# Performance work log

Hardware: AMD Instinct MI355X
Metric: run time of the kernel (lower is better)

Reference implementation:

```python
import jax, jax.numpy as jnp
import numpy as np

N, D, K = 32768, 256, 8192
SQRT3 = 3.0 ** 0.5


def setup_inputs() -> dict:
    key = jax.random.key(0)
    k1, k2 = jax.random.split(key)
    x = jax.random.normal(k1, (N, D), dtype=jnp.float32)
    # torch .uniform_(-sqrt(3), sqrt(3)) on an [D, K] table
    embeddings = jax.random.uniform(k2, (D, K), dtype=jnp.float32,
                                    minval=-SQRT3, maxval=SQRT3)
    return {"x": x, "embeddings": embeddings}


def reference(x, embeddings):
    # x: [N, D] (forward flattens from dim 1; 2D input is identity)
    # embeddings: [D, K]
    # squared L2 distances: ||y||^2 - 2 y.E + ||e||^2  -> [N, K]
    dist = (jnp.sum(x * x, axis=1, keepdims=True)
            - 2.0 * (x @ embeddings)
            + jnp.sum(embeddings * embeddings, axis=0, keepdims=True))
    idx = jnp.argmin(dist, axis=1)  # [N]
    # one_hot(idx) @ E^T == gather of columns of E (same math, no dense one-hot)
    quantized = jnp.take(embeddings, idx, axis=1).T  # [N, D]
    return quantized.reshape(x.shape)
```

## Files before the change

### kernel.cpp

```cpp
#include <hip/hip_runtime.h>
#include <math.h>
#include <float.h>

#define N_ROWS 32768
#define D_DIM  256
#define K_DIM  8192

#define EPS1 0.25f
#define EPS2 0.02f
#define T2CAP 4096
#define T3CAP 512
#define NSPLIT3 16

typedef _Float16 f16;
typedef _Float16 f16x8 __attribute__((ext_vector_type(8)));
typedef float f32x4 __attribute__((ext_vector_type(4)));

#define KSPLIT 8
#define COLS_PER_SPLIT (K_DIM / KSPLIT)
#define CHUNK_COLS 32
#define NCHUNK (COLS_PER_SPLIT / CHUNK_COLS)

__global__ void convx_kernel(const float* __restrict__ X, f16* __restrict__ X16) {
    const size_t i = ((size_t)blockIdx.x * 256 + threadIdx.x) * 8;
    float4 a = *reinterpret_cast<const float4*>(X + i);
    float4 b = *reinterpret_cast<const float4*>(X + i + 4);
    f16x8 o;
    o[0]=(f16)a.x; o[1]=(f16)a.y; o[2]=(f16)a.z; o[3]=(f16)a.w;
    o[4]=(f16)b.x; o[5]=(f16)b.y; o[6]=(f16)b.z; o[7]=(f16)b.w;
    *reinterpret_cast<f16x8*>(X16 + i) = o;
}

__global__ void transpose_kernel(const float* __restrict__ E, float* __restrict__ ET) {
    __shared__ float t[64][65];
    const int bk = blockIdx.x & (K_DIM / 64 - 1);
    const int bd = blockIdx.x >> 7;
    const int c  = threadIdx.x & 63;
    const int r0 = (threadIdx.x >> 6) * 16;
    const int d0 = bd * 64, k0 = bk * 64;
#pragma unroll
    for (int i = 0; i < 16; ++i)
        t[r0 + i][c] = E[(size_t)(d0 + r0 + i) * K_DIM + k0 + c];
    __syncthreads();
#pragma unroll
    for (int i = 0; i < 16; ++i)
        ET[(size_t)(k0 + r0 + i) * D_DIM + d0 + c] = t[c][r0 + i];
}

__global__ void packe_et_kernel(const float* __restrict__ ET, f16* __restrict__ Epack) {
    const int gid = blockIdx.x * 256 + threadIdx.x;
    const int l    = gid & 63;
    const int t    = (gid >> 6) & 7;
    const int tile = gid >> 9;
    const int k  = 16 * tile + (l & 15);
    const int d0 = 32 * t + (l >> 4) * 8;
    float4 a = *reinterpret_cast<const float4*>(&ET[(size_t)k * D_DIM + d0]);
    float4 b = *reinterpret_cast<const float4*>(&ET[(size_t)k * D_DIM + d0 + 4]);
    f16x8 o;
    o[0]=(f16)a.x; o[1]=(f16)a.y; o[2]=(f16)a.z; o[3]=(f16)a.w;
    o[4]=(f16)b.x; o[5]=(f16)b.y; o[6]=(f16)b.z; o[7]=(f16)b.w;
    *reinterpret_cast<f16x8*>(Epack + (size_t)gid * 8) = o;
}

__global__ void packe_kernel(const float* __restrict__ E, f16* __restrict__ Epack) {
    const int gid = blockIdx.x * 256 + threadIdx.x;
    const int l    = gid & 63;
    const int t    = (gid >> 6) & 7;
    const int tile = gid >> 9;
    const int k  = 16 * tile + (l & 15);
    const int d0 = 32 * t + (l >> 4) * 8;
    f16x8 o;
#pragma unroll
    for (int j = 0; j < 8; ++j) o[j] = (f16)E[(size_t)(d0 + j) * K_DIM + k];
    *reinterpret_cast<f16x8*>(Epack + (size_t)gid * 8) = o;
}

__global__ void nhen_kernel(const float* __restrict__ E, float* __restrict__ nhen) {
    const int k = blockIdx.x * 256 + threadIdx.x;
    float s = 0.0f;
#pragma unroll 8
    for (int d = 0; d < D_DIM; ++d) {
        float v = E[(size_t)d * K_DIM + k];
        s = fmaf(v, v, s);
    }
    nhen[k] = -0.5f * s;
}

__launch_bounds__(256, 2)
__global__ void pass1_kernel(const f16* __restrict__ X16,
                             const f16* __restrict__ Epack,
                             const float* __restrict__ nhen,
                             float* __restrict__ p_best,
                             float* __restrict__ p_sec,
                             int*   __restrict__ p_idx) {
    __shared__ f16 B_lds[2][8192];

    const int tid = threadIdx.x;
    const int wv = tid >> 6;
    const int lane = tid & 63;
    const int l15 = lane & 15;
    const int l4  = lane >> 4;
    const int rg = blockIdx.x >> 3;
    const int ks = blockIdx.x & 7;
    const int rowW = rg * 256 + wv * 64;
    const int colBase = ks * COLS_PER_SPLIT;

    f16x8 A[4][8];
#pragma unroll
    for (int rt = 0; rt < 4; ++rt)
#pragma unroll
        for (int t = 0; t < 8; ++t)
            A[rt][t] = *reinterpret_cast<const f16x8*>(
                X16 + (size_t)(rowW + 16*rt + l15) * D_DIM + 32*t + l4*8);

    float best[16], sec[16];
    int bbase[16];
#pragma unroll
    for (int s = 0; s < 16; ++s) { best[s] = -INFINITY; sec[s] = -INFINITY; bbase[s] = 0; }

    const float4* src = reinterpret_cast<const float4*>(
        Epack + (size_t)colBase * 256);

    float4 sreg[4];
#pragma unroll
    for (int q = 0; q < 4; ++q) sreg[q] = src[q*256 + tid];
    {
        float4* bw = reinterpret_cast<float4*>(&B_lds[0][0]);
#pragma unroll
        for (int q = 0; q < 4; ++q) bw[q*256 + tid] = sreg[q];
    }

    for (int ci = 0; ci < NCHUNK; ++ci) {
        __syncthreads();
        if (ci + 1 < NCHUNK) {
#pragma unroll
            for (int q = 0; q < 4; ++q)
                sreg[q] = src[(size_t)(ci+1)*1024 + q*256 + tid];
        }
        const f16* bufc = &B_lds[ci & 1][0];
        const int c0 = colBase + ci * CHUNK_COLS;

#pragma unroll
        for (int ct = 0; ct < 2; ++ct) {
            const float nh = nhen[c0 + 16*ct + l15];
            const f32x4 nh4 = {nh, nh, nh, nh};
            f32x4 acc[4];
            {
                f16x8 B = *reinterpret_cast<const f16x8*>(bufc + (ct*8)*512 + lane*8);
#pragma unroll
                for (int rt = 0; rt < 4; ++rt)
                    acc[rt] = __builtin_amdgcn_mfma_f32_16x16x32_f16(A[rt][0], B, nh4, 0, 0, 0);
            }
#pragma unroll
            for (int t = 1; t < 8; ++t) {
                f16x8 B = *reinterpret_cast<const f16x8*>(bufc + (ct*8 + t)*512 + lane*8);
#pragma unroll
                for (int rt = 0; rt < 4; ++rt)
                    acc[rt] = __builtin_amdgcn_mfma_f32_16x16x32_f16(A[rt][t], B, acc[rt], 0, 0, 0);
            }
#pragma unroll
            for (int rt = 0; rt < 4; ++rt) {
#pragma unroll
                for (int r = 0; r < 4; ++r) {
                    const float v = acc[rt][r];
                    const int sl = rt*4 + r;
                    sec[sl] = __builtin_amdgcn_fmed3f(v, best[sl], sec[sl]);
                    const bool gt = v > best[sl];
                    best[sl] = gt ? v : best[sl];
                    bbase[sl] = gt ? (c0 + 16*ct) : bbase[sl];
                }
            }
        }

        if (ci + 1 < NCHUNK) {
            float4* bw = reinterpret_cast<float4*>(&B_lds[(ci+1) & 1][0]);
#pragma unroll
            for (int q = 0; q < 4; ++q) bw[q*256 + tid] = sreg[q];
        }
    }

#pragma unroll
    for (int s = 0; s < 16; ++s) {
        float b = best[s], sc = sec[s];
        int k = bbase[s] + l15;
#pragma unroll
        for (int off = 8; off >= 1; off >>= 1) {
            float ob = __shfl_xor(b, off, 16);
            float os = __shfl_xor(sc, off, 16);
            int   ok = __shfl_xor(k, off, 16);
            float sm = fmaxf(fmaxf(sc, os), fminf(b, ob));
            bool take = (ob > b) || (ob == b && ok < k);
            b = take ? ob : b;
            k = take ? ok : k;
            sc = sm;
        }
        if (l15 == 0) {
            const int row = rowW + 16*(s >> 2) + 4*l4 + (s & 3);
            p_best[ks * N_ROWS + row] = b;
            p_sec [ks * N_ROWS + row] = sc;
            p_idx [ks * N_ROWS + row] = k;
        }
    }
}

__global__ void zero_counts_kernel(int* count, int* count3) { *count = 0; *count3 = 0; }

__global__ void merge_kernel(const float* __restrict__ p_best,
                             const float* __restrict__ p_sec,
                             const int*   __restrict__ p_idx,
                             int* __restrict__ idxf,
                             int* __restrict__ list, int* __restrict__ count) {
    const int n = blockIdx.x * 256 + threadIdx.x;
    float b = p_best[n], sc = p_sec[n];
    int k = p_idx[n];
#pragma unroll
    for (int s = 1; s < KSPLIT; ++s) {
        float ob = p_best[s * N_ROWS + n];
        float os = p_sec [s * N_ROWS + n];
        int   ok = p_idx [s * N_ROWS + n];
        float sm = fmaxf(fmaxf(sc, os), fminf(b, ob));
        bool take = ob > b;
        b = take ? ob : b; k = take ? ok : k; sc = sm;
    }
    idxf[n] = k;
    if (2.0f * (b - sc) < EPS1) {
        int pos = atomicAdd(count, 1);
        if (pos < T2CAP) list[pos] = n;
    }
}

__launch_bounds__(256, 2)
__global__ void tier2_kernel(const float* __restrict__ X,
                             const float* __restrict__ E,
                             const float* __restrict__ nhen,
                             const int* __restrict__ list,
                             const int* __restrict__ count,
                             float* __restrict__ t2b, float* __restrict__ t2s,
                             int* __restrict__ t2i) {
    const int g  = blockIdx.x >> 4;
    const int sp = blockIdx.x & 15;
    const int cnt = min(*count, T2CAP);
    if (g * 64 >= cnt) return;

    __shared__ float xT[D_DIM][64];
    __shared__ float es[64][64];
    const int tid = threadIdx.x;
    const int tx = tid & 15, ty = tid >> 4;

    {
        const int r = tid >> 2;
        const int slot = min(g * 64 + r, cnt - 1);
        const int row = list[slot];
        const int d0 = (tid & 3) * 64;
        const float* xp = X + (size_t)row * D_DIM + d0;
#pragma unroll
        for (int i = 0; i < 64; i += 4) {
            float4 v = *reinterpret_cast<const float4*>(xp + i);
            xT[d0+i+0][r] = v.x; xT[d0+i+1][r] = v.y;
            xT[d0+i+2][r] = v.z; xT[d0+i+3][r] = v.w;
        }
    }

    float best[4], sec[4]; int bidx[4];
#pragma unroll
    for (int i = 0; i < 4; ++i) { best[i] = -INFINITY; sec[i] = -INFINITY; bidx[i] = 0; }

    const int colBase = sp * 512;
    for (int kc = 0; kc < 512; kc += 64) {
        float acc[4][4];
#pragma unroll
        for (int i = 0; i < 4; ++i)
#pragma unroll
            for (int j = 0; j < 4; ++j) acc[i][j] = 0.0f;

        for (int dc = 0; dc < D_DIM; dc += 64) {
            __syncthreads();
#pragma unroll
            for (int dd = 0; dd < 64; dd += 16) {
                int d = dd + (tid >> 4);
                float4 v = *reinterpret_cast<const float4*>(
                    &E[(size_t)(dc + d) * K_DIM + colBase + kc + (tid & 15) * 4]);
                *reinterpret_cast<float4*>(&es[d][(tid & 15) * 4]) = v;
            }
            __syncthreads();
#pragma unroll 8
            for (int d = 0; d < 64; ++d) {
                float4 xv = *reinterpret_cast<const float4*>(&xT[dc + d][ty * 4]);
                float4 ev = *reinterpret_cast<const float4*>(&es[d][tx * 4]);
                float xr[4] = {xv.x, xv.y, xv.z, xv.w};
                float ec[4] = {ev.x, ev.y, ev.z, ev.w};
#pragma unroll
                for (int i = 0; i < 4; ++i)
#pragma unroll
                    for (int j = 0; j < 4; ++j)
                        acc[i][j] = fmaf(xr[i], ec[j], acc[i][j]);
            }
        }
        float4 nhv = *reinterpret_cast<const float4*>(&nhen[colBase + kc + tx * 4]);
        float nh[4] = {nhv.x, nhv.y, nhv.z, nhv.w};
#pragma unroll
        for (int j = 0; j < 4; ++j) {
            const int k = colBase + kc + tx * 4 + j;
#pragma unroll
            for (int i = 0; i < 4; ++i) {
                float u = nh[j] + acc[i][j];
                bool gt = u > best[i];
                sec[i]  = fmaxf(sec[i], fminf(u, best[i]));
                best[i] = gt ? u : best[i];
                bidx[i] = gt ? k : bidx[i];
            }
        }
    }

#pragma unroll
    for (int off = 8; off >= 1; off >>= 1) {
#pragma unroll
        for (int i = 0; i < 4; ++i) {
            float ob = __shfl_xor(best[i], off, 16);
            float os = __shfl_xor(sec[i], off, 16);
            int   ok = __shfl_xor(bidx[i], off, 16);
            float sm = fmaxf(fmaxf(sec[i], os), fminf(best[i], ob));
            bool take = (ob > best[i]) || (ob == best[i] && ok < bidx[i]);
            best[i] = take ? ob : best[i];
            bidx[i] = take ? ok : bidx[i];
            sec[i] = sm;
        }
    }
    if (tx == 0) {
#pragma unroll
        for (int i = 0; i < 4; ++i) {
            const int slot = g * 64 + ty * 4 + i;
            if (slot < cnt) {
                t2b[sp * T2CAP + slot] = best[i];
                t2s[sp * T2CAP + slot] = sec[i];
                t2i[sp * T2CAP + slot] = bidx[i];
            }
        }
    }
}

__global__ void merge2_kernel(const float* __restrict__ t2b,
                              const float* __restrict__ t2s,
                              const int*   __restrict__ t2i,
                              const int* __restrict__ list,
                              const int* __restrict__ count,
                              int* __restrict__ idxf,
                              int* __restrict__ list3, int* __restrict__ count3) {
    const int slot = blockIdx.x * 256 + threadIdx.x;
    const int cnt = min(*count, T2CAP);
    if (slot >= cnt) return;
    float b = t2b[slot], sc = t2s[slot];
    int k = t2i[slot];
#pragma unroll
    for (int sp = 1; sp < 16; ++sp) {
        float ob = t2b[sp * T2CAP + slot];
        float os = t2s[sp * T2CAP + slot];
        int   ok = t2i[sp * T2CAP + slot];
        float sm = fmaxf(fmaxf(sc, os), fminf(b, ob));
        bool take = ob > b;
        b = take ? ob : b; k = take ? ok : k; sc = sm;
    }
    const int n = list[slot];
    idxf[n] = k;
    if (2.0f * (b - sc) < EPS2) {
        int pos = atomicAdd(count3, 1);
        if (pos < T3CAP) list3[pos] = n;
    }
}

__launch_bounds__(256)
__global__ void tier3_kernel(const float* __restrict__ X,
                             const float* __restrict__ E,
                             const int* __restrict__ list3,
                             const int* __restrict__ count3,
                             double* __restrict__ t3b, int* __restrict__ t3i) {
    const int slot = blockIdx.x >> 4;
    const int sp   = blockIdx.x & 15;
    const int cnt = min(*count3, T3CAP);
    if (slot >= cnt) return;
    const int n = list3[slot];

    __shared__ float xs[D_DIM];
    const int tid = threadIdx.x;
    xs[tid] = X[(size_t)n * D_DIM + tid];
    __syncthreads();

    const int colBase = sp * 512;
    double best = DBL_MAX;
    int bi = 0x7fffffff;
#pragma unroll
    for (int kk = 0; kk < 512; kk += 256) {
        const int k = colBase + kk + tid;
        double s0 = 0.0, s1 = 0.0, s2 = 0.0, s3 = 0.0;
#pragma unroll 4
        for (int d = 0; d < D_DIM; d += 4) {
            double f0 = (double)xs[d+0] - (double)E[(size_t)(d+0) * K_DIM + k];
            double f1 = (double)xs[d+1] - (double)E[(size_t)(d+1) * K_DIM + k];
            double f2 = (double)xs[d+2] - (double)E[(size_t)(d+2) * K_DIM + k];
            double f3 = (double)xs[d+3] - (double)E[(size_t)(d+3) * K_DIM + k];
            s0 = fma(f0, f0, s0); s1 = fma(f1, f1, s1);
            s2 = fma(f2, f2, s2); s3 = fma(f3, f3, s3);
        }
        double s = (s0 + s1) + (s2 + s3);
        if (s < best) { best = s; bi = k; }
    }

    __shared__ double bv[256];
    __shared__ int bix[256];
    bv[tid] = best; bix[tid] = bi;
    __syncthreads();
    if (tid == 0) {
        double b = bv[0]; int ix = bix[0];
        for (int t = 1; t < 256; ++t)
            if (bv[t] < b || (bv[t] == b && bix[t] < ix)) { b = bv[t]; ix = bix[t]; }
        t3b[sp * T3CAP + slot] = b;
        t3i[sp * T3CAP + slot] = ix;
    }
}

__global__ void merge3_kernel(const double* __restrict__ t3b,
                              const int* __restrict__ t3i,
                              const int* __restrict__ list3,
                              const int* __restrict__ count3,
                              int* __restrict__ idxf) {
    const int slot = blockIdx.x * 256 + threadIdx.x;
    const int cnt = min(*count3, T3CAP);
    if (slot >= cnt) return;
    double b = t3b[slot];
    int k = t3i[slot];
#pragma unroll
    for (int sp = 1; sp < NSPLIT3; ++sp) {
        double ob = t3b[sp * T3CAP + slot];
        int   ok = t3i[sp * T3CAP + slot];
        if (ob < b || (ob == b && ok < k)) { b = ob; k = ok; }
    }
    idxf[list3[slot]] = k;
}

__global__ void gather2_kernel(const float* __restrict__ ET,
                               const int* __restrict__ idx,
                               float* __restrict__ out) {
    const int n  = blockIdx.x * 4 + (threadIdx.x >> 6);
    const int d4 = (threadIdx.x & 63) * 4;
    const int k  = idx[n];
    *reinterpret_cast<float4*>(&out[(size_t)n * D_DIM + d4]) =
        *reinterpret_cast<const float4*>(&ET[(size_t)k * D_DIM + d4]);
}

__global__ void gather_kernel(const float* __restrict__ E,
                              const int* __restrict__ idx,
                              float* __restrict__ out) {
    const int n = blockIdx.x;
    const int d = threadIdx.x;
    const int k = idx[n];
    out[(size_t)n * D_DIM + d] = E[(size_t)d * K_DIM + k];
}

__global__ void fb_enorm_kernel(const float* __restrict__ E, float* __restrict__ enorm) {
    int k = blockIdx.x * 256 + threadIdx.x;
    float s = 0.0f;
#pragma unroll 8
    for (int d = 0; d < D_DIM; ++d) { float v = E[(size_t)d * K_DIM + k]; s = fmaf(v, v, s); }
    enorm[k] = s;
}

__launch_bounds__(256, 2)
__global__ void fb_dist_kernel(const float* __restrict__ X, const float* __restrict__ E,
                               const float* __restrict__ enorm,
                               int* __restrict__ idx_out, float* __restrict__ gap_out) {
    __shared__ float xT[D_DIM][64];
    __shared__ float es[64][64];
    const int tid = threadIdx.x;
    const int tx = tid & 15, ty = tid >> 4;
    const int rowBase = blockIdx.x * 64;
    {
        const int r = tid >> 2;
        const int d0 = (tid & 3) * 64;
        const float* xp = X + (size_t)(rowBase + r) * D_DIM + d0;
#pragma unroll
        for (int i = 0; i < 64; i += 4) {
            float4 v = *reinterpret_cast<const float4*>(xp + i);
            xT[d0+i+0][r]=v.x; xT[d0+i+1][r]=v.y; xT[d0+i+2][r]=v.z; xT[d0+i+3][r]=v.w;
        }
    }
    float bestVal[4], secVal[4]; int bestIdx[4];
#pragma unroll
    for (int i = 0; i < 4; ++i) { bestVal[i]=INFINITY; secVal[i]=INFINITY; bestIdx[i]=0; }
    for (int kc = 0; kc < K_DIM; kc += 64) {
        float acc[4][4];
#pragma unroll
        for (int i=0;i<4;++i)
#pragma unroll
            for (int j=0;j<4;++j) acc[i][j]=0.f;
        for (int dc = 0; dc < D_DIM; dc += 64) {
            __syncthreads();
#pragma unroll
            for (int dd = 0; dd < 64; dd += 16) {
                int d = dd + (tid >> 4);
                float4 v = *reinterpret_cast<const float4*>(
                    &E[(size_t)(dc+d)*K_DIM + kc + (tid&15)*4]);
                *reinterpret_cast<float4*>(&es[d][(tid&15)*4]) = v;
            }
            __syncthreads();
#pragma unroll 8
            for (int d = 0; d < 64; ++d) {
                float4 xv = *reinterpret_cast<const float4*>(&xT[dc+d][ty*4]);
                float4 ev = *reinterpret_cast<const float4*>(&es[d][tx*4]);
                float xr[4]={xv.x,xv.y,xv.z,xv.w}, ec[4]={ev.x,ev.y,ev.z,ev.w};
#pragma unroll
                for (int i=0;i<4;++i)
#pragma unroll
                    for (int j=0;j<4;++j) acc[i][j]=fmaf(xr[i],ec[j],acc[i][j]);
            }
        }
        float4 env = *reinterpret_cast<const float4*>(&enorm[kc + tx*4]);
        float en[4]={env.x,env.y,env.z,env.w};
#pragma unroll
        for (int j=0;j<4;++j) {
            int k = kc + tx*4 + j;
#pragma unroll
            for (int i=0;i<4;++i) {
                float s = fmaf(-2.0f, acc[i][j], en[j]);
                if (s < bestVal[i]) { secVal[i]=bestVal[i]; bestVal[i]=s; bestIdx[i]=k; }
                else if (s < secVal[i]) secVal[i]=s;
            }
        }
    }
#pragma unroll
    for (int off=8; off>=1; off>>=1) {
#pragma unroll
        for (int i=0;i<4;++i) {
            float oB=__shfl_xor(bestVal[i],off,16);
            int oI=__shfl_xor(bestIdx[i],off,16);
            float oS=__shfl_xor(secVal[i],off,16);
            float ms=fminf(fminf(secVal[i],oS),fmaxf(bestVal[i],oB));
            if (oB<bestVal[i] || (oB==bestVal[i] && oI<bestIdx[i])) { bestVal[i]=oB; bestIdx[i]=oI; }
            secVal[i]=ms;
        }
    }
    if (tx==0) {
#pragma unroll
        for (int i=0;i<4;++i) {
            idx_out[rowBase + ty*4 + i] = bestIdx[i];
            gap_out[rowBase + ty*4 + i] = secVal[i]-bestVal[i];
        }
    }
}

__launch_bounds__(256)
__global__ void fb_refine_kernel(const float* __restrict__ X, const float* __restrict__ E,
                                 const float* __restrict__ gap, int* __restrict__ idx) {
    const int n = blockIdx.x;
    if (gap[n] >= 0.0625f) return;
    __shared__ float xs[D_DIM];
    const int tid = threadIdx.x;
    xs[tid] = X[(size_t)n * D_DIM + tid];
    __syncthreads();
    double best = DBL_MAX; int bi = 0x7fffffff;
    for (int k = tid; k < K_DIM; k += 256) {
        double s0=0,s1=0,s2=0,s3=0;
#pragma unroll 4
        for (int d = 0; d < D_DIM; d += 4) {
            double f0=(double)xs[d+0]-(double)E[(size_t)(d+0)*K_DIM+k];
            double f1=(double)xs[d+1]-(double)E[(size_t)(d+1)*K_DIM+k];
            double f2=(double)xs[d+2]-(double)E[(size_t)(d+2)*K_DIM+k];
            double f3=(double)xs[d+3]-(double)E[(size_t)(d+3)*K_DIM+k];
            s0=fma(f0,f0,s0); s1=fma(f1,f1,s1); s2=fma(f2,f2,s2); s3=fma(f3,f3,s3);
        }
        double s=(s0+s1)+(s2+s3);
        if (s<best){best=s;bi=k;}
    }
    __shared__ double bv[256]; __shared__ int bix[256];
    bv[tid]=best; bix[tid]=bi;
    __syncthreads();
    if (tid==0) {
        double b=bv[0]; int ix=bix[0];
        for (int t=1;t<256;++t)
            if (bv[t]<b || (bv[t]==b && bix[t]<ix)) { b=bv[t]; ix=bix[t]; }
        idx[n]=ix;
    }
}

extern "C" void kernel_launch(void* const* d_in, const int* in_sizes, int n_in,
                              void* d_out, int out_size, void* d_ws, size_t ws_size,
                              hipStream_t stream) {
    const float* X = (const float*)d_in[0];
    const float* E = (const float*)d_in[1];
    float* out = (float*)d_out;
    char* ws = (char*)d_ws;

    const size_t o_nhen  = 0;
    const size_t o_pb    = 32768;
    const size_t o_ps    = o_pb  + (size_t)KSPLIT * N_ROWS * 4;
    const size_t o_pi    = o_ps  + (size_t)KSPLIT * N_ROWS * 4;
    const size_t o_idx   = o_pi  + (size_t)KSPLIT * N_ROWS * 4;
    const size_t o_list  = o_idx + (size_t)N_ROWS * 4;
    const size_t o_count = o_list + (size_t)T2CAP * 4;
    const size_t o_t2b   = o_count + 256;
    const size_t o_t2s   = o_t2b + (size_t)16 * T2CAP * 4;
    const size_t o_t2i   = o_t2s + (size_t)16 * T2CAP * 4;
    const size_t o_list3 = o_t2i + (size_t)16 * T2CAP * 4;
    const size_t o_t3b   = o_list3 + (size_t)T3CAP * 4;
    const size_t o_t3i   = o_t3b + (size_t)NSPLIT3 * T3CAP * 8;
    const size_t o_x16   = o_t3i + (size_t)NSPLIT3 * T3CAP * 4;
    const size_t o_epack = o_x16 + (size_t)N_ROWS * D_DIM * 2;
    const size_t NEED_BASE = o_epack + (size_t)D_DIM * K_DIM * 2;
    const size_t o_et    = NEED_BASE;
    const size_t NEED_FULL = o_et + (size_t)D_DIM * K_DIM * 4;

    if (ws_size >= NEED_BASE) {
        float*  nhen  = (float*) (ws + o_nhen);
        float*  p_b   = (float*) (ws + o_pb);
        float*  p_s   = (float*) (ws + o_ps);
        int*    p_i   = (int*)   (ws + o_pi);
        int*    idxf  = (int*)   (ws + o_idx);
        int*    list  = (int*)   (ws + o_list);
        int*    count = (int*)   (ws + o_count);
        int*    count3= (int*)   (ws + o_count + 4);
        float*  t2b   = (float*) (ws + o_t2b);
        float*  t2s   = (float*) (ws + o_t2s);
        int*    t2i   = (int*)   (ws + o_t2i);
        int*    list3 = (int*)   (ws + o_list3);
        double* t3b   = (double*)(ws + o_t3b);
        int*    t3i   = (int*)   (ws + o_t3i);
        f16*    X16   = (f16*)   (ws + o_x16);
        f16*    Epack = (f16*)   (ws + o_epack);
        float*  ET    = (float*) (ws + o_et);
        const bool haveET = ws_size >= NEED_FULL;

        convx_kernel<<<(N_ROWS * D_DIM / 8) / 256, 256, 0, stream>>>(X, X16);
        if (haveET) {
            transpose_kernel<<<(K_DIM / 64) * (D_DIM / 64), 256, 0, stream>>>(E, ET);
            packe_et_kernel<<<(K_DIM / 16) * 8 * 64 / 256, 256, 0, stream>>>(ET, Epack);
        } else {
            packe_kernel<<<(K_DIM / 16) * 8 * 64 / 256, 256, 0, stream>>>(E, Epack);
        }
        nhen_kernel<<<K_DIM / 256, 256, 0, stream>>>(E, nhen);
        zero_counts_kernel<<<1, 1, 0, stream>>>(count, count3);
        pass1_kernel<<<(N_ROWS / 256) * KSPLIT, 256, 0, stream>>>(
            X16, Epack, nhen, p_b, p_s, p_i);
        merge_kernel<<<N_ROWS / 256, 256, 0, stream>>>(
            p_b, p_s, p_i, idxf, list, count);
        tier2_kernel<<<(T2CAP / 64) * 16, 256, 0, stream>>>(
            X, E, nhen, list, count, t2b, t2s, t2i);
        merge2_kernel<<<T2CAP / 256, 256, 0, stream>>>(
            t2b, t2s, t2i, list, count, idxf, list3, count3);
        tier3_kernel<<<T3CAP * NSPLIT3, 256, 0, stream>>>(
            X, E, list3, count3, t3b, t3i);
        merge3_kernel<<<T3CAP / 256, 256, 0, stream>>>(
            t3b, t3i, list3, count3, idxf);
        if (haveET)
            gather2_kernel<<<N_ROWS / 4, 256, 0, stream>>>(ET, idxf, out);
        else
            gather_kernel<<<N_ROWS, 256, 0, stream>>>(E, idxf, out);
    } else {
        float* enorm = (float*)ws;
        int*   idx   = (int*)(ws + 32768);
        float* gap   = (float*)(ws + 32768 + (size_t)N_ROWS * 4);
        fb_enorm_kernel<<<K_DIM / 256, 256, 0, stream>>>(E, enorm);
        fb_dist_kernel<<<N_ROWS / 64, 256, 0, stream>>>(X, E, enorm, idx, gap);
        fb_refine_kernel<<<N_ROWS, 256, 0, stream>>>(X, E, gap, idx);
        gather_kernel<<<N_ROWS, 256, 0, stream>>>(E, idx, out);
    }
}
```

Before: 327.7 us.

## Triple-buffer codebook chunks with direct global-to-LDS async loads in pass1

Replaces the register-staged double-buffered copy of codebook chunks into LDS with direct global_load_lds transfers into a three-deep LDS ring. Loads run two chunks ahead and are gated by vmcnt waits plus raw barriers. The per-column norm terms are also preloaded once into LDS instead of being read from global memory per chunk. This is meant to free VGPRs, remove the LDS write instructions and hide load latency, at the cost of more LDS and fragile manual waitcnt/barrier ordering.

```diff
diff --git a/kernel.cpp b/kernel.cpp
--- a/kernel.cpp
+++ b/kernel.cpp
@@ -20,6 +20,14 @@
 #define COLS_PER_SPLIT (K_DIM / KSPLIT)
 #define CHUNK_COLS 32
 #define NCHUNK (COLS_PER_SPLIT / CHUNK_COLS)
+#define CHUNK_BYTES (CHUNK_COLS * D_DIM * 2)
+
+typedef unsigned int u32;
+typedef const u32 __attribute__((address_space(1)))* gas1_u32;
+typedef u32 __attribute__((address_space(3)))* las3_u32;
+__device__ __forceinline__ void gload_lds16(const void* g, void* l) {
+    __builtin_amdgcn_global_load_lds((gas1_u32)g, (las3_u32)l, 16, 0, 0);
+}
 
 __global__ void convx_kernel(const float* __restrict__ X, f16* __restrict__ X16) {
     const size_t i = ((size_t)blockIdx.x * 256 + threadIdx.x) * 8;
@@ -93,7 +101,8 @@
                              float* __restrict__ p_best,
                              float* __restrict__ p_sec,
                              int*   __restrict__ p_idx) {
-    __shared__ f16 B_lds[2][8192];
+    __shared__ f16 B_lds[3][CHUNK_BYTES / 2];
+    __shared__ float nh_lds[COLS_PER_SPLIT];
 
     const int tid = threadIdx.x;
     const int wv = tid >> 6;
@@ -113,36 +122,32 @@
             A[rt][t] = *reinterpret_cast<const f16x8*>(
                 X16 + (size_t)(rowW + 16*rt + l15) * D_DIM + 32*t + l4*8);
 
+    *reinterpret_cast<float4*>(&nh_lds[tid * 4]) =
+        *reinterpret_cast<const float4*>(nhen + colBase + tid * 4);
+
     float best[16], sec[16];
     int bbase[16];
 #pragma unroll
     for (int s = 0; s < 16; ++s) { best[s] = -INFINITY; sec[s] = -INFINITY; bbase[s] = 0; }
 
-    const float4* src = reinterpret_cast<const float4*>(
-        Epack + (size_t)colBase * 256);
-
-    float4 sreg[4];
-#pragma unroll
-    for (int q = 0; q < 4; ++q) sreg[q] = src[q*256 + tid];
-    {
-        float4* bw = reinterpret_cast<float4*>(&B_lds[0][0]);
-#pragma unroll
-        for (int q = 0; q < 4; ++q) bw[q*256 + tid] = sreg[q];
-    }
-
-    for (int ci = 0; ci < NCHUNK; ++ci) {
-        __syncthreads();
-        if (ci + 1 < NCHUNK) {
-#pragma unroll
-            for (int q = 0; q < 4; ++q)
-                sreg[q] = src[(size_t)(ci+1)*1024 + q*256 + tid];
-        }
-        const f16* bufc = &B_lds[ci & 1][0];
+    const char* splitSrc = (const char*)Epack + (size_t)colBase * 512;
+
+    auto STAGE = [&](int buf, int ci) {
+        const char* csrc = splitSrc + (size_t)ci * CHUNK_BYTES;
+        char* cdst = (char*)&B_lds[buf][0];
+#pragma unroll
+        for (int c = 0; c < 4; ++c) {
+            const int seg = wv * 4 + c;
+            gload_lds16(csrc + seg * 1024 + (lane << 4), cdst + seg * 1024);
+        }
+    };
+
+    auto COMPUTE = [&](int bi, int ci) {
+        const f16* bufc = &B_lds[bi][0];
         const int c0 = colBase + ci * CHUNK_COLS;
-
 #pragma unroll
         for (int ct = 0; ct < 2; ++ct) {
-            const float nh = nhen[c0 + 16*ct + l15];
+            const float nh = nh_lds[ci * CHUNK_COLS + ct * 16 + l15];
             const f32x4 nh4 = {nh, nh, nh, nh};
             f32x4 acc[4];
             {
@@ -171,13 +176,26 @@
                 }
             }
         }
-
-        if (ci + 1 < NCHUNK) {
-            float4* bw = reinterpret_cast<float4*>(&B_lds[(ci+1) & 1][0]);
-#pragma unroll
-            for (int q = 0; q < 4; ++q) bw[q*256 + tid] = sreg[q];
-        }
-    }
+    };
+
+    STAGE(0, 0);
+    STAGE(1, 1);
+    asm volatile("s_waitcnt lgkmcnt(0)" ::: "memory");
+
+    int cur = 0;
+    for (int ci = 0; ci < NCHUNK - 1; ++ci) {
+        asm volatile("s_waitcnt vmcnt(4)" ::: "memory");
+        __builtin_amdgcn_s_barrier();
+        if (ci + 2 < NCHUNK) {
+            int nb = cur + 2; if (nb >= 3) nb -= 3;
+            STAGE(nb, ci + 2);
+        }
+        COMPUTE(cur, ci);
+        cur = (cur + 1 == 3) ? 0 : cur + 1;
+    }
+    asm volatile("s_waitcnt vmcnt(0)" ::: "memory");
+    __builtin_amdgcn_s_barrier();
+    COMPUTE(cur, NCHUNK - 1);
 
 #pragma unroll
     for (int s = 0; s < 16; ++s) {
```

Result: no change. 325.2 us (-0.8%).
